# Kernel tuning notes

Measured on AMD Instinct MI355X. Metric: run time of the kernel, lower is better.

## Reference

```python
import math
import jax, jax.numpy as jnp
import numpy as np

B, T, HIDDEN = 2, 2048, 1024
H, HKV, D = 16, 16, 64


def _rope_tables(T, D):
    inv_freq = 1.0 / (10000.0 ** (jnp.arange(0, D, 2, dtype=jnp.float32) / D))
    t = jnp.arange(T, dtype=jnp.float32)
    freqs = jnp.outer(t, inv_freq)               # [T, D/2]
    emb = jnp.concatenate([freqs, freqs], axis=-1)  # [T, D]
    return jnp.cos(emb), jnp.sin(emb)


def setup_inputs() -> dict:
    key = jax.random.key(0)
    k1, k2, k3 = jax.random.split(key, 3)
    hidden_states = jax.random.normal(k1, (B, T, HIDDEN), dtype=jnp.float32)
    cos, sin = _rope_tables(T, D)
    # trunc-normal-ish init, std = 1/sqrt(fan_in)
    w_qkv = jax.random.normal(k2, ((H + 2 * HKV) * D, HIDDEN), dtype=jnp.float32) / math.sqrt(HIDDEN)
    w_o = jax.random.normal(k3, (HIDDEN, H * D), dtype=jnp.float32) / math.sqrt(H * D)
    return {"hidden_states": hidden_states, "cos": cos, "sin": sin, "w_qkv": w_qkv, "w_o": w_o}


def _rotate_half(x):
    x1, x2 = jnp.split(x, 2, axis=-1)
    return jnp.concatenate([-x2, x1], axis=-1)


def reference(hidden_states, cos, sin, w_qkv, w_o):
    b, t, _ = hidden_states.shape
    # fused QKV projection: [B,T,(H+2*HKV)*D]
    qkv = jnp.einsum('bti,oi->bto', hidden_states, w_qkv)
    qkv = qkv.reshape(b, t, H + 2 * HKV, D)
    q = qkv[:, :, :H]                    # [B,T,H,D]
    k = qkv[:, :, H:H + HKV]             # [B,T,HKV,D]
    v = qkv[:, :, H + HKV:]              # [B,T,HKV,D]
    # inline RoPE; cos/sin broadcast over heads
    c = cos[:, None, :]
    s = sin[:, None, :]
    q = q * c + _rotate_half(q) * s
    k = k * c + _rotate_half(k) * s
    scale = 1.0 / math.sqrt(D)
    attn_scores = jnp.einsum('bthd,bThd->bhtT', q, k) * scale  # [B,H,T,T]
    mask = jnp.tril(jnp.ones((t, t), dtype=bool))
    attn_scores = jnp.where(mask[None, None, :, :], attn_scores, -1e9)
    attn = jax.nn.softmax(attn_scores, axis=-1)
    context = jnp.einsum('bhtT,bThd->bthd', attn, v).reshape(b, t, H * D)
    return jnp.einsum('bti,oi->bto', context, w_o)
```

## Files before the change

kernel.cpp:

```cpp
#include <hip/hip_runtime.h>

typedef __bf16 bf16_t;
typedef __bf16 bf16x4 __attribute__((ext_vector_type(4)));
typedef __bf16 bf16x8 __attribute__((ext_vector_type(8)));
typedef float f32x4 __attribute__((ext_vector_type(4)));
typedef unsigned int u32x2 __attribute__((ext_vector_type(2)));
typedef unsigned long long u64;

#define MFMA16(a, b, c) __builtin_amdgcn_mfma_f32_16x16x32_bf16((a), (b), (c), 0, 0, 0)

#define LDG2LDS16(g, l)                                                        \
    __builtin_amdgcn_global_load_lds(                                          \
        (const __attribute__((address_space(1))) void*)(g),                    \
        (__attribute__((address_space(3))) void*)(l), 16, 0, 0)

#if __has_builtin(__builtin_amdgcn_exp2f)
#define EXP2(x) __builtin_amdgcn_exp2f(x)
#else
#define EXP2(x) exp2f(x)
#endif

__device__ inline bf16x8 load8(const float* p) {
    const f32x4 a = *(const f32x4*)p;
    const f32x4 b = *(const f32x4*)(p + 4);
    bf16x8 r;
#pragma unroll
    for (int i = 0; i < 4; i++) { r[i] = (bf16_t)a[i]; r[4 + i] = (bf16_t)b[i]; }
    return r;
}

__device__ inline u32x2 as2(bf16x4 v) {
    u32x2 r;
    __builtin_memcpy(&r, &v, 8);
    return r;
}

__device__ inline bf16x4 shfl4(bf16x4 v, int src) {
    u64 x;
    __builtin_memcpy(&x, &v, 8);
    x = __shfl(x, src, 64);
    bf16x4 r;
    __builtin_memcpy(&r, &x, 8);
    return r;
}

__global__ __launch_bounds__(256) void convert_kernel(const float* __restrict__ hs,
                                                      const float* __restrict__ wqkv,
                                                      const float* __restrict__ wo,
                                                      bf16_t* __restrict__ outb) {
    const size_t c = ((size_t)blockIdx.x * 256 + threadIdx.x) * 8;
    const float* src;
    size_t off;
    if (c < 4194304) { src = hs; off = c; }
    else if (c < 7340032) { src = wqkv; off = c - 4194304; }
    else { src = wo; off = c - 7340032; }
    *(bf16x8*)(outb + c) = load8(src + off);
}


template <int MODE, int NDIM, int BM>
__global__ __launch_bounds__(256) void gemm_bt(const bf16_t* __restrict__ A,
                                               const bf16_t* __restrict__ B,
                                               float* __restrict__ outp,
                                               bf16_t* __restrict__ q_ws,
                                               bf16_t* __restrict__ k_ws,
                                               bf16_t* __restrict__ v_ws,
                                               const float* __restrict__ cosb,
                                               const float* __restrict__ sinb) {
    constexpr int K = 1024;
    constexpr int IM = BM / 32;
    __shared__ __align__(16) bf16_t As[BM * 32];
    __shared__ __align__(16) bf16_t Bs[128 * 32];

    const int tid = threadIdx.x;
    const int w = tid >> 6;
    const int lane = tid & 63;
    const int lr = lane & 15;
    const int quad = lane >> 4;
    const int m0 = blockIdx.y * BM;
    const int n0 = blockIdx.x * 128;
    const int wm = (w & 1) * (BM / 2);
    const int wn = (w >> 1) * 64;

    const int srow = tid >> 2;
    const int skk = (((tid & 3) ^ ((tid >> 3) & 3)) * 8);
    const bf16_t* gA0 = A + (size_t)(m0 + srow) * K + skk;
    const bf16_t* gA1 = gA0 + (size_t)64 * K;
    const bf16_t* gB0 = B + (size_t)(n0 + srow) * K + skk;
    const bf16_t* gB1 = gB0 + (size_t)64 * K;
    bf16_t* lA0 = As + w * 512;
    bf16_t* lA1 = As + 2048 + w * 512;
    bf16_t* lB0 = Bs + w * 512;
    bf16_t* lB1 = Bs + 2048 + w * 512;

    const int qsw = (quad ^ ((lr >> 1) & 3)) * 8;

    f32x4 acc[IM][4] = {};

    for (int k0 = 0; k0 < K; k0 += 32) {
        LDG2LDS16(gA0 + k0, lA0);
        if constexpr (BM == 128) LDG2LDS16(gA1 + k0, lA1);
        LDG2LDS16(gB0 + k0, lB0);
        LDG2LDS16(gB1 + k0, lB1);
        __syncthreads();

        bf16x8 af[IM], bfm[4];
#pragma unroll
        for (int im = 0; im < IM; im++)
            af[im] = *(const bf16x8*)&As[(wm + im * 16 + lr) * 32 + qsw];
#pragma unroll
        for (int in = 0; in < 4; in++)
            bfm[in] = *(const bf16x8*)&Bs[(wn + in * 16 + lr) * 32 + qsw];
#pragma unroll
        for (int im = 0; im < IM; im++)
#pragma unroll
            for (int in = 0; in < 4; in++)
                acc[im][in] = MFMA16(af[im], bfm[in], acc[im][in]);
        __syncthreads();
    }

    if constexpr (MODE == 0) {
#pragma unroll
        for (int im = 0; im < IM; im++)
#pragma unroll
            for (int in = 0; in < 4; in++)
#pragma unroll
                for (int r = 0; r < 4; r++) {
                    const int m = m0 + wm + im * 16 + quad * 4 + r;
                    const int n = n0 + wn + in * 16 + lr;
                    outp[(size_t)m * NDIM + n] = acc[im][in][r];
                }
    } else {
        const int j = (n0 + wn) >> 6;
        if (j < 32) {
            const bool isq = (j < 16);
            const float qs = 0.125f * 1.44269504089f;
#pragma unroll
            for (int im = 0; im < IM; im++) {
#pragma unroll
                for (int r = 0; r < 4; r++) {
                    const int m = m0 + wm + im * 16 + quad * 4 + r;
                    const int b = m >> 11;
                    const int t = m & 2047;
#pragma unroll
                    for (int in = 0; in < 2; in++) {
                        const int d = in * 16 + lr;
                        const float x1 = acc[im][in][r];
                        const float x2 = acc[im][in + 2][r];
                        const float c = cosb[t * 64 + d];
                        const float s = sinb[t * 64 + d];
                        float y1 = x1 * c - x2 * s;
                        float y2 = x2 * c + x1 * s;
                        if (isq) {
                            y1 *= qs; y2 *= qs;
                            const size_t base =
                                ((size_t)(b * 16 + j) * 2048 + t) * 64 + d;
                            q_ws[base] = (bf16_t)y1;
                            q_ws[base + 32] = (bf16_t)y2;
                        } else {
                            const int bh = b * 16 + (j - 16);
                            const size_t off =
                                ((size_t)(bh * 128 + (t >> 4)) * 2) * 512 +
                                ((t & 15) + (d >> 3) * 16) * 8 + (d & 7);
                            k_ws[off] = (bf16_t)y1;
                            k_ws[off + 512] = (bf16_t)y2;
                        }
                    }
                }
            }
        } else {
#pragma unroll
            for (int im = 0; im < IM; im++)
#pragma unroll
                for (int in = 0; in < 4; in++)
#pragma unroll
                    for (int r = 0; r < 4; r++) {
                        const int m = m0 + wm + im * 16 + quad * 4 + r;
                        const int b = m >> 11;
                        const int t = m & 2047;
                        const int d = in * 16 + lr;
                        const int bh = b * 16 + (j - 32);
                        const size_t off =
                            ((size_t)(bh * 64 + (t >> 5)) * 4 + (d >> 4)) * 512 +
                            ((d & 15) + ((t & 31) >> 3) * 16) * 8 + (t & 7);
                        v_ws[off] = (bf16_t)acc[im][in][r];
                    }
        }
    }
}

__global__ __launch_bounds__(256) void attn_kernel(const bf16_t* __restrict__ q_ws,
                                                   const bf16_t* __restrict__ k_ws,
                                                   const bf16_t* __restrict__ v_ws,
                                                   bf16_t* __restrict__ ctx) {
    __shared__ __align__(16) bf16_t Ks[2][4096];
    __shared__ __align__(16) bf16_t Vs[2][4096];

    const int tid = threadIdx.x;
    const int w = tid >> 6;
    const int lane = tid & 63;
    const int lr = lane & 15;
    const int quad = lane >> 4;
    const int bh = blockIdx.x & 31;
    const int pr = blockIdx.x >> 5;
    const int b = bh >> 4;
    const int hd = bh & 15;

    const bf16_t* kws = k_ws + (size_t)bh * 131072;
    const bf16_t* vws = v_ws + (size_t)bh * 131072;
    const int soff = w * 512 + lane * 8;
    const int lo8 = lane * 8;

#define ASTAGE(kb, buf)                                                        \
    {                                                                          \
        LDG2LDS16(kws + (size_t)(kb) * 4096 + soff, &Ks[buf][w * 512]);        \
        LDG2LDS16(kws + (size_t)(kb) * 4096 + 2048 + soff,                     \
                  &Ks[buf][2048 + w * 512]);                                   \
        LDG2LDS16(vws + (size_t)(kb) * 4096 + soff, &Vs[buf][w * 512]);        \
        LDG2LDS16(vws + (size_t)(kb) * 4096 + 2048 + soff,                     \
                  &Vs[buf][2048 + w * 512]);                                   \
    }

#pragma unroll
    for (int half = 0; half < 2; half++) {
        const int qt = half ? (31 - pr) : pr;
        const int trow = qt * 64 + w * 16;
        const int query = trow + lr;

        const bf16_t* qb = q_ws + ((size_t)bh * 2048 + trow + lr) * 64 + quad * 8;
        const bf16x8 qlo = *(const bf16x8*)qb;
        const bf16x8 qhi = *(const bf16x8*)(qb + 32);

        f32x4 o[4] = {};
        float lrun = 0.0f;

        ASTAGE(0, 0);
        asm volatile("s_waitcnt vmcnt(0)" ::: "memory");
        __builtin_amdgcn_s_barrier();
        asm volatile("" ::: "memory");

        for (int kb = 0; kb <= qt; kb++) {
            const int buf = kb & 1;
            if (kb < qt) ASTAGE(kb + 1, buf ^ 1);

            f32x4 s[4];
#pragma unroll
            for (int n = 0; n < 4; n++) {
                const bf16x8 k0 = *(const bf16x8*)&Ks[buf][(2 * n) * 512 + lo8];
                const bf16x8 k1 = *(const bf16x8*)&Ks[buf][(2 * n + 1) * 512 + lo8];
                const f32x4 z = {};
                s[n] = MFMA16(k0, qlo, z);
                s[n] = MFMA16(k1, qhi, s[n]);
            }

            const int u0 = kb * 64;
            if (kb == qt) {
#pragma unroll
                for (int n = 0; n < 4; n++)
#pragma unroll
                    for (int r = 0; r < 4; r++)
                        if (u0 + n * 16 + quad * 4 + r > query) s[n][r] = -1e9f;
            }

            f32x4 p[4];
#pragma unroll
            for (int n = 0; n < 4; n++)
#pragma unroll
                for (int r = 0; r < 4; r++) p[n][r] = EXP2(s[n][r]);

            lrun += ((p[0][0] + p[0][1]) + (p[0][2] + p[0][3])) +
                    ((p[1][0] + p[1][1]) + (p[1][2] + p[1][3])) +
                    ((p[2][0] + p[2][1]) + (p[2][2] + p[2][3])) +
                    ((p[3][0] + p[3][1]) + (p[3][2] + p[3][3]));

            bf16x4 pb[4];
#pragma unroll
            for (int n = 0; n < 4; n++)
#pragma unroll
                for (int r = 0; r < 4; r++) pb[n][r] = (bf16_t)p[n][r];

#pragma unroll
            for (int hh = 0; hh < 2; hh++) {
                bf16x8 pf;
#if __has_builtin(__builtin_amdgcn_permlane16_swap) && \
    __has_builtin(__builtin_amdgcn_permlane32_swap)
                const u32x2 P0 = as2(pb[2 * hh]);
                const u32x2 P1 = as2(pb[2 * hh + 1]);
                const u32x2 s1a = __builtin_amdgcn_permlane16_swap(P0[0], P0[1], false, false);
                const u32x2 s1b = __builtin_amdgcn_permlane16_swap(P1[0], P1[1], false, false);
                const u32x2 s2a = __builtin_amdgcn_permlane32_swap(s1a[0], s1b[0], false, false);
                const u32x2 s2b = __builtin_amdgcn_permlane32_swap(s1a[1], s1b[1], false, false);
                const u32x2 s3a = __builtin_amdgcn_permlane16_swap(s2a[0], s2a[1], false, false);
                const u32x2 s3b = __builtin_amdgcn_permlane16_swap(s2b[0], s2b[1], false, false);
                const unsigned pfd[4] = {s3a[0], s3a[1], s3b[0], s3b[1]};
                __builtin_memcpy(&pf, pfd, 16);
#else
                const int srcLow = ((quad & 1) << 5) + lr;
                const int srcHigh = srcLow + 16;
                const bool loSel = (quad < 2);
                const bf16x4 a0 = shfl4(pb[2 * hh], srcLow);
                const bf16x4 a1 = shfl4(pb[2 * hh + 1], srcLow);
                const bf16x4 b0 = shfl4(pb[2 * hh], srcHigh);
                const bf16x4 b1 = shfl4(pb[2 * hh + 1], srcHigh);
                const bf16x4 lo = loSel ? a0 : a1;
                const bf16x4 hi = loSel ? b0 : b1;
#pragma unroll
                for (int r = 0; r < 4; r++) { pf[r] = lo[r]; pf[4 + r] = hi[r]; }
#endif
#pragma unroll
                for (int n = 0; n < 4; n++) {
                    const bf16x8 vvf =
                        *(const bf16x8*)&Vs[buf][(hh * 4 + n) * 512 + lo8];
                    o[n] = MFMA16(vvf, pf, o[n]);
                }
            }

            asm volatile("s_waitcnt lgkmcnt(0) vmcnt(0)" ::: "memory");
            __builtin_amdgcn_s_barrier();
            asm volatile("" ::: "memory");
        }

        lrun += __shfl_xor(lrun, 16);
        lrun += __shfl_xor(lrun, 32);

        const float inv = 1.0f / fmaxf(lrun, 1e-30f);
        const size_t base = ((size_t)b * 2048 + query) * 1024 + hd * 64 + quad * 4;
#pragma unroll
        for (int n = 0; n < 4; n++) {
            bf16x4 ob;
#pragma unroll
            for (int r = 0; r < 4; r++) ob[r] = (bf16_t)(o[n][r] * inv);
            *(bf16x4*)&ctx[base + n * 16] = ob;
        }
    }
#undef ASTAGE
}

extern "C" void kernel_launch(void* const* d_in, const int* in_sizes, int n_in,
                              void* d_out, int out_size, void* d_ws, size_t ws_size,
                              hipStream_t stream) {
    const float* hs = (const float*)d_in[0];
    const float* cosb = (const float*)d_in[1];
    const float* sinb = (const float*)d_in[2];
    const float* wqkv = (const float*)d_in[3];
    const float* wo = (const float*)d_in[4];
    float* out = (float*)d_out;

    char* ws = (char*)d_ws;
    bf16_t* hs_b = (bf16_t*)(ws);
    bf16_t* wqkv_b = hs_b + 4194304;
    bf16_t* wo_b = hs_b + 7340032;
    bf16_t* q_ws = (bf16_t*)(ws + (size_t)(16u << 20));
    bf16_t* k_ws = (bf16_t*)(ws + (size_t)(24u << 20));
    bf16_t* v_ws = (bf16_t*)(ws + (size_t)(32u << 20));
    bf16_t* ctx = (bf16_t*)(ws);

    const dim3 blk(256);

    convert_kernel<<<dim3(4096), blk, 0, stream>>>(hs, wqkv, wo, hs_b);

    gemm_bt<1, 3072, 128><<<dim3(24, 32), blk, 0, stream>>>(
        hs_b, wqkv_b, nullptr, q_ws, k_ws, v_ws, cosb, sinb);

    attn_kernel<<<dim3(512), blk, 0, stream>>>(q_ws, k_ws, v_ws, ctx);

    gemm_bt<0, 1024, 64><<<dim3(8, 64), blk, 0, stream>>>(
        ctx, wo_b, out, nullptr, nullptr, nullptr, nullptr, nullptr);
}
```

Before: 172.9 us.

## Fuse paired causal query tiles into one K/V sweep and remap block order

The attention kernel used to process its two query tiles (pr and 31-pr) one after the other, streaming K/V twice. Now both tiles share a single pass over key blocks: each loaded K/V tile feeds MFMAs for both queries, and tile A stops contributing once past its diagonal. Block indexing also changes so that consecutive blocks share the same batch-head, with pr remapped to interleave short and long work. This cuts LDS staging traffic and barriers, at the cost of higher register pressure from two accumulator sets.

```diff
diff --git a/kernel.cpp b/kernel.cpp
--- a/kernel.cpp
+++ b/kernel.cpp
@@ -42,6 +42,36 @@
     bf16x4 r;
     __builtin_memcpy(&r, &x, 8);
     return r;
+}
+
+__device__ inline bf16x8 p2pf(bf16x4 pb0, bf16x4 pb1, int quad, int lr) {
+    bf16x8 pf;
+#if __has_builtin(__builtin_amdgcn_permlane16_swap) && \
+    __has_builtin(__builtin_amdgcn_permlane32_swap)
+    const u32x2 P0 = as2(pb0);
+    const u32x2 P1 = as2(pb1);
+    const u32x2 s1a = __builtin_amdgcn_permlane16_swap(P0[0], P0[1], false, false);
+    const u32x2 s1b = __builtin_amdgcn_permlane16_swap(P1[0], P1[1], false, false);
+    const u32x2 s2a = __builtin_amdgcn_permlane32_swap(s1a[0], s1b[0], false, false);
+    const u32x2 s2b = __builtin_amdgcn_permlane32_swap(s1a[1], s1b[1], false, false);
+    const u32x2 s3a = __builtin_amdgcn_permlane16_swap(s2a[0], s2a[1], false, false);
+    const u32x2 s3b = __builtin_amdgcn_permlane16_swap(s2b[0], s2b[1], false, false);
+    const unsigned pfd[4] = {s3a[0], s3a[1], s3b[0], s3b[1]};
+    __builtin_memcpy(&pf, pfd, 16);
+#else
+    const int srcLow = ((quad & 1) << 5) + lr;
+    const int srcHigh = srcLow + 16;
+    const bool loSel = (quad < 2);
+    const bf16x4 a0 = shfl4(pb0, srcLow);
+    const bf16x4 a1 = shfl4(pb1, srcLow);
+    const bf16x4 b0 = shfl4(pb0, srcHigh);
+    const bf16x4 b1 = shfl4(pb1, srcHigh);
+    const bf16x4 lo = loSel ? a0 : a1;
+    const bf16x4 hi = loSel ? b0 : b1;
+#pragma unroll
+    for (int r = 0; r < 4; r++) { pf[r] = lo[r]; pf[4 + r] = hi[r]; }
+#endif
+    return pf;
 }
 
 __global__ __launch_bounds__(256) void convert_kernel(const float* __restrict__ hs,
@@ -201,8 +231,11 @@
     const int lane = tid & 63;
     const int lr = lane & 15;
     const int quad = lane >> 4;
-    const int bh = blockIdx.x & 31;
-    const int pr = blockIdx.x >> 5;
+    const int bh = blockIdx.x >> 4;
+    const int p = blockIdx.x & 15;
+    const int pr = (p < 8) ? p : 23 - p;
+    const int qtA = pr;
+    const int qtB = 31 - pr;
     const int b = bh >> 4;
     const int hd = bh & 15;
 
@@ -221,117 +254,140 @@
                   &Vs[buf][2048 + w * 512]);                                   \
     }
 
-#pragma unroll
-    for (int half = 0; half < 2; half++) {
-        const int qt = half ? (31 - pr) : pr;
-        const int trow = qt * 64 + w * 16;
-        const int query = trow + lr;
-
-        const bf16_t* qb = q_ws + ((size_t)bh * 2048 + trow + lr) * 64 + quad * 8;
-        const bf16x8 qlo = *(const bf16x8*)qb;
-        const bf16x8 qhi = *(const bf16x8*)(qb + 32);
-
-        f32x4 o[4] = {};
-        float lrun = 0.0f;
-
-        ASTAGE(0, 0);
-        asm volatile("s_waitcnt vmcnt(0)" ::: "memory");
+    const int queryA = qtA * 64 + w * 16 + lr;
+    const int queryB = qtB * 64 + w * 16 + lr;
+
+    const bf16_t* qbA = q_ws + ((size_t)bh * 2048 + queryA) * 64 + quad * 8;
+    const bf16_t* qbB = q_ws + ((size_t)bh * 2048 + queryB) * 64 + quad * 8;
+    const bf16x8 qloA = *(const bf16x8*)qbA;
+    const bf16x8 qhiA = *(const bf16x8*)(qbA + 32);
+    const bf16x8 qloB = *(const bf16x8*)qbB;
+    const bf16x8 qhiB = *(const bf16x8*)(qbB + 32);
+
+    f32x4 oA[4] = {}, oB[4] = {};
+    float lrA = 0.0f, lrB = 0.0f;
+
+    ASTAGE(0, 0);
+    asm volatile("s_waitcnt vmcnt(0)" ::: "memory");
+    __builtin_amdgcn_s_barrier();
+    asm volatile("" ::: "memory");
+
+    for (int kb = 0; kb <= qtB; kb++) {
+        const int buf = kb & 1;
+        if (kb < qtB) ASTAGE(kb + 1, buf ^ 1);
+
+        const bool actA = (kb <= qtA);
+        const int u0 = kb * 64;
+
+        bf16x8 kf[8];
+#pragma unroll
+        for (int n = 0; n < 4; n++) {
+            kf[2 * n] = *(const bf16x8*)&Ks[buf][(2 * n) * 512 + lo8];
+            kf[2 * n + 1] = *(const bf16x8*)&Ks[buf][(2 * n + 1) * 512 + lo8];
+        }
+
+        f32x4 sB[4];
+#pragma unroll
+        for (int n = 0; n < 4; n++) {
+            const f32x4 z = {};
+            sB[n] = MFMA16(kf[2 * n], qloB, z);
+            sB[n] = MFMA16(kf[2 * n + 1], qhiB, sB[n]);
+        }
+        f32x4 sA[4];
+        if (actA) {
+#pragma unroll
+            for (int n = 0; n < 4; n++) {
+                const f32x4 z = {};
+                sA[n] = MFMA16(kf[2 * n], qloA, z);
+                sA[n] = MFMA16(kf[2 * n + 1], qhiA, sA[n]);
+            }
+        }
+
+        if (kb == qtB) {
+#pragma unroll
+            for (int n = 0; n < 4; n++)
+#pragma unroll
+                for (int r = 0; r < 4; r++)
+                    if (u0 + n * 16 + quad * 4 + r > queryB) sB[n][r] = -1e9f;
+        }
+        if (kb == qtA) {
+#pragma unroll
+            for (int n = 0; n < 4; n++)
+#pragma unroll
+                for (int r = 0; r < 4; r++)
+                    if (u0 + n * 16 + quad * 4 + r > queryA) sA[n][r] = -1e9f;
+        }
+
+        bf16x4 pbB[4], pbA[4];
+        {
+            f32x4 pB[4];
+#pragma unroll
+            for (int n = 0; n < 4; n++)
+#pragma unroll
+                for (int r = 0; r < 4; r++) pB[n][r] = EXP2(sB[n][r]);
+            lrB += ((pB[0][0] + pB[0][1]) + (pB[0][2] + pB[0][3])) +
+                   ((pB[1][0] + pB[1][1]) + (pB[1][2] + pB[1][3])) +
+                   ((pB[2][0] + pB[2][1]) + (pB[2][2] + pB[2][3])) +
+                   ((pB[3][0] + pB[3][1]) + (pB[3][2] + pB[3][3]));
+#pragma unroll
+            for (int n = 0; n < 4; n++)
+#pragma unroll
+                for (int r = 0; r < 4; r++) pbB[n][r] = (bf16_t)pB[n][r];
+        }
+        if (actA) {
+            f32x4 pA[4];
+#pragma unroll
+            for (int n = 0; n < 4; n++)
+#pragma unroll
+                for (int r = 0; r < 4; r++) pA[n][r] = EXP2(sA[n][r]);
+            lrA += ((pA[0][0] + pA[0][1]) + (pA[0][2] + pA[0][3])) +
+                   ((pA[1][0] + pA[1][1]) + (pA[1][2] + pA[1][3])) +
+                   ((pA[2][0] + pA[2][1]) + (pA[2][2] + pA[2][3])) +
+                   ((pA[3][0] + pA[3][1]) + (pA[3][2] + pA[3][3]));
+#pragma unroll
+            for (int n = 0; n < 4; n++)
+#pragma unroll
+                for (int r = 0; r < 4; r++) pbA[n][r] = (bf16_t)pA[n][r];
+        }
+
+#pragma unroll
+        for (int hh = 0; hh < 2; hh++) {
+            const bf16x8 pfB = p2pf(pbB[2 * hh], pbB[2 * hh + 1], quad, lr);
+            bf16x8 pfA;
+            if (actA) pfA = p2pf(pbA[2 * hh], pbA[2 * hh + 1], quad, lr);
+#pragma unroll
+            for (int n = 0; n < 4; n++) {
+                const bf16x8 vvf =
+                    *(const bf16x8*)&Vs[buf][(hh * 4 + n) * 512 + lo8];
+                oB[n] = MFMA16(vvf, pfB, oB[n]);
+                if (actA) oA[n] = MFMA16(vvf, pfA, oA[n]);
+            }
+        }
+
+        asm volatile("s_waitcnt lgkmcnt(0) vmcnt(0)" ::: "memory");
         __builtin_amdgcn_s_barrier();
         asm volatile("" ::: "memory");
-
-        for (int kb = 0; kb <= qt; kb++) {
-            const int buf = kb & 1;
-            if (kb < qt) ASTAGE(kb + 1, buf ^ 1);
-
-            f32x4 s[4];
-#pragma unroll
-            for (int n = 0; n < 4; n++) {
-                const bf16x8 k0 = *(const bf16x8*)&Ks[buf][(2 * n) * 512 + lo8];
-                const bf16x8 k1 = *(const bf16x8*)&Ks[buf][(2 * n + 1) * 512 + lo8];
-                const f32x4 z = {};
-                s[n] = MFMA16(k0, qlo, z);
-                s[n] = MFMA16(k1, qhi, s[n]);
-            }
-
-            const int u0 = kb * 64;
-            if (kb == qt) {
-#pragma unroll
-                for (int n = 0; n < 4; n++)
-#pragma unroll
-                    for (int r = 0; r < 4; r++)
-                        if (u0 + n * 16 + quad * 4 + r > query) s[n][r] = -1e9f;
-            }
-
-            f32x4 p[4];
-#pragma unroll
-            for (int n = 0; n < 4; n++)
-#pragma unroll
-                for (int r = 0; r < 4; r++) p[n][r] = EXP2(s[n][r]);
-
-            lrun += ((p[0][0] + p[0][1]) + (p[0][2] + p[0][3])) +
-                    ((p[1][0] + p[1][1]) + (p[1][2] + p[1][3])) +
-                    ((p[2][0] + p[2][1]) + (p[2][2] + p[2][3])) +
-                    ((p[3][0] + p[3][1]) + (p[3][2] + p[3][3]));
-
-            bf16x4 pb[4];
-#pragma unroll
-            for (int n = 0; n < 4; n++)
-#pragma unroll
-                for (int r = 0; r < 4; r++) pb[n][r] = (bf16_t)p[n][r];
-
-#pragma unroll
-            for (int hh = 0; hh < 2; hh++) {
-                bf16x8 pf;
-#if __has_builtin(__builtin_amdgcn_permlane16_swap) && \
-    __has_builtin(__builtin_amdgcn_permlane32_swap)
-                const u32x2 P0 = as2(pb[2 * hh]);
-                const u32x2 P1 = as2(pb[2 * hh + 1]);
-                const u32x2 s1a = __builtin_amdgcn_permlane16_swap(P0[0], P0[1], false, false);
-                const u32x2 s1b = __builtin_amdgcn_permlane16_swap(P1[0], P1[1], false, false);
-                const u32x2 s2a = __builtin_amdgcn_permlane32_swap(s1a[0], s1b[0], false, false);
-                const u32x2 s2b = __builtin_amdgcn_permlane32_swap(s1a[1], s1b[1], false, false);
-                const u32x2 s3a = __builtin_amdgcn_permlane16_swap(s2a[0], s2a[1], false, false);
-                const u32x2 s3b = __builtin_amdgcn_permlane16_swap(s2b[0], s2b[1], false, false);
-                const unsigned pfd[4] = {s3a[0], s3a[1], s3b[0], s3b[1]};
-                __builtin_memcpy(&pf, pfd, 16);
-#else
-                const int srcLow = ((quad & 1) << 5) + lr;
-                const int srcHigh = srcLow + 16;
-                const bool loSel = (quad < 2);
-                const bf16x4 a0 = shfl4(pb[2 * hh], srcLow);
-                const bf16x4 a1 = shfl4(pb[2 * hh + 1], srcLow);
-                const bf16x4 b0 = shfl4(pb[2 * hh], srcHigh);
-                const bf16x4 b1 = shfl4(pb[2 * hh + 1], srcHigh);
-                const bf16x4 lo = loSel ? a0 : a1;
-                const bf16x4 hi = loSel ? b0 : b1;
-#pragma unroll
-                for (int r = 0; r < 4; r++) { pf[r] = lo[r]; pf[4 + r] = hi[r]; }
-#endif
-#pragma unroll
-                for (int n = 0; n < 4; n++) {
-                    const bf16x8 vvf =
-                        *(const bf16x8*)&Vs[buf][(hh * 4 + n) * 512 + lo8];
-                    o[n] = MFMA16(vvf, pf, o[n]);
-                }
-            }
-
-            asm volatile("s_waitcnt lgkmcnt(0) vmcnt(0)" ::: "memory");
-            __builtin_amdgcn_s_barrier();
-            asm volatile("" ::: "memory");
-        }
-
-        lrun += __shfl_xor(lrun, 16);
-        lrun += __shfl_xor(lrun, 32);
-
-        const float inv = 1.0f / fmaxf(lrun, 1e-30f);
-        const size_t base = ((size_t)b * 2048 + query) * 1024 + hd * 64 + quad * 4;
-#pragma unroll
-        for (int n = 0; n < 4; n++) {
-            bf16x4 ob;
-#pragma unroll
-            for (int r = 0; r < 4; r++) ob[r] = (bf16_t)(o[n][r] * inv);
-            *(bf16x4*)&ctx[base + n * 16] = ob;
-        }
+    }
+
+    lrA += __shfl_xor(lrA, 16);
+    lrA += __shfl_xor(lrA, 32);
+    lrB += __shfl_xor(lrB, 16);
+    lrB += __shfl_xor(lrB, 32);
+
+    const float invA = 1.0f / fmaxf(lrA, 1e-30f);
+    const float invB = 1.0f / fmaxf(lrB, 1e-30f);
+    const size_t baseA = ((size_t)b * 2048 + queryA) * 1024 + hd * 64 + quad * 4;
+    const size_t baseB = ((size_t)b * 2048 + queryB) * 1024 + hd * 64 + quad * 4;
+#pragma unroll
+    for (int n = 0; n < 4; n++) {
+        bf16x4 obA, obB;
+#pragma unroll
+        for (int r = 0; r < 4; r++) {
+            obA[r] = (bf16_t)(oA[n][r] * invA);
+            obB[r] = (bf16_t)(oB[n][r] * invB);
+        }
+        *(bf16x4*)&ctx[baseA + n * 16] = obA;
+        *(bf16x4*)&ctx[baseB + n * 16] = obB;
     }
 #undef ASTAGE
 }
```

Result: slower. 192.7 us (+11.4%).
